# Optimization experiments

Measured on AMD Instinct MI355X. Metric: run time of the kernel, lower is better.

The kernel has to match this reference:

```python
import jax, jax.numpy as jnp
import numpy as np

B = 8            # graphs per batch
NUM_DNA = 2048   # DNA nodes per graph (equal across batch, as the module requires)
NPG = NUM_DNA + 2  # +2 contact nodes at the start of each graph
N = B * NPG
HID = 128


def _build_edges():
    # Each undirected DNA-DNA pair appears exactly once (src < dst), matching the
    # processed_pairs dedup in the torch reference. Offsets 1..4 -> ~4 couplings/node.
    rows, cols = [], []
    for b in range(B):
        base = b * NPG + 2
        for d in range(1, 5):
            i = np.arange(NUM_DNA - d)
            rows.append(base + i)
            cols.append(base + i + d)
    return np.stack([np.concatenate(rows), np.concatenate(cols)]).astype(np.int32)


def setup_inputs() -> dict:
    key = jax.random.key(0)
    ks = jax.random.split(key, 12)
    edge_index = jnp.asarray(_build_edges())          # [2, 65456]
    E = edge_index.shape[1]
    batch = jnp.repeat(jnp.arange(B, dtype=jnp.int32), NPG)  # [N]
    # contacts = first 2 nodes per graph, all-zero original features
    onf = jax.random.uniform(ks[0], (N, 4), jnp.float32) + 0.1
    contact_idx = (jnp.arange(B) * NPG)[:, None] + jnp.arange(2)[None, :]
    onf = onf.at[contact_idx.reshape(-1)].set(0.0)
    s = 1.0 / np.sqrt(HID)
    return {
        "node_features": jax.random.normal(ks[1], (N, HID), jnp.float32),
        "edge_features": jax.random.normal(ks[2], (E, HID), jnp.float32),
        "original_node_features": onf,
        "Wo1": jax.random.normal(ks[3], (HID, HID), jnp.float32) * s,
        "bo1": jax.random.normal(ks[4], (HID,), jnp.float32) * 0.01,
        "Wo2": jax.random.normal(ks[5], (HID, 1), jnp.float32) * s,
        "bo2": jax.random.normal(ks[6], (1,), jnp.float32) * 0.01,
        "Wc1": jax.random.normal(ks[7], (HID, HID), jnp.float32) * s,
        "bc1": jax.random.normal(ks[8], (HID,), jnp.float32) * 0.01,
        "Wc2": jax.random.normal(ks[9], (HID, 1), jnp.float32) * s,
        "bc2": jax.random.normal(ks[10], (1,), jnp.float32) * 0.01,
        "edge_index": edge_index,
        "batch": batch,
        "batch_size": B,
        "num_dna_nodes": NUM_DNA,
    }


def reference(node_features, edge_features, original_node_features,
              Wo1, bo1, Wo2, bo2, Wc1, bc1, Wc2, bc2,
              edge_index, batch, batch_size, num_dna_nodes):
    # Vectorized construct_hamiltonian_from_graph with n_orb = 1.
    n_orb = 1
    H_size = num_dna_nodes * n_orb
    contact = jnp.all(original_node_features == 0, axis=1)
    dna_mask = ~contact
    node_counts = jax.ops.segment_sum(jnp.ones_like(batch), batch,
                                      num_segments=batch_size)
    graph_starts = jnp.concatenate([jnp.zeros((1,), node_counts.dtype),
                                    jnp.cumsum(node_counts)[:-1]])
    # DNA node bookkeeping (contacts are the first 2 nodes of each graph)
    dna_idx = jnp.nonzero(dna_mask, size=batch_size * num_dna_nodes,
                          fill_value=0)[0]
    dna_batch = batch[dna_idx]
    dna_local = dna_idx - graph_starts[dna_batch] - 2
    # onsite MLP: Linear -> ReLU -> Linear, Hermitize (identity for n_orb=1)
    dna_feat = node_features[dna_idx]
    onsite = jax.nn.relu(dna_feat @ Wo1 + bo1) @ Wo2 + bo2      # [Nd, 1]
    coupling = jax.nn.relu(edge_features @ Wc1 + bc1) @ Wc2 + bc2  # [E, 1]
    # edge -> (graph, local row/col), upper-triangular orientation u <= v
    src, dst = edge_index[0], edge_index[1]
    eb = batch[src]
    src_loc = src - graph_starts[eb] - 2
    dst_loc = dst - graph_starts[eb] - 2
    u = jnp.minimum(src_loc, dst_loc)
    v = jnp.maximum(src_loc, dst_loc)
    valid = dna_mask[src] & dna_mask[dst] & (u != v)
    c = coupling[:, 0] * valid.astype(coupling.dtype)
    Hm = jnp.zeros((batch_size, H_size, H_size), jnp.float32)
    Hm = Hm.at[dna_batch, dna_local, dna_local].set(onsite[:, 0])
    Hm = Hm.at[eb, u, v].add(c)   # each undirected pair appears once -> add == set
    Hm = Hm.at[eb, v, u].add(c)   # Hermitian mirror (real, 1x1 blocks)
    Hm = Hm + 1e-6 * jnp.eye(H_size, dtype=Hm.dtype)
    return Hm
```

## Files before the change

### kernel.cpp

```cpp
#include <hip/hip_runtime.h>
#include <hip/hip_bf16.h>

#define HID   128
#define NPG   2050
#define HSZ   2048
#define WSTR  136

typedef __attribute__((ext_vector_type(8))) short bf16x8;
typedef __attribute__((ext_vector_type(4))) float f32x4;

union BF8 { bf16x8 v; __hip_bfloat162 h[4]; };

__device__ __forceinline__ bf16x8 cvt8(const float4 x0, const float4 x1) {
    BF8 r;
    r.h[0] = __float22bfloat162_rn(make_float2(x0.x, x0.y));
    r.h[1] = __float22bfloat162_rn(make_float2(x0.z, x0.w));
    r.h[2] = __float22bfloat162_rn(make_float2(x1.x, x1.y));
    r.h[3] = __float22bfloat162_rn(make_float2(x1.z, x1.w));
    return r.v;
}

__global__ __launch_bounds__(256) void mlp_mfma_kernel(
    const float* __restrict__ node_features,
    const float* __restrict__ edge_features,
    const float* __restrict__ Wo1, const float* __restrict__ bo1,
    const float* __restrict__ Wo2, const float* __restrict__ bo2,
    const float* __restrict__ Wc1, const float* __restrict__ bc1,
    const float* __restrict__ Wc2, const float* __restrict__ bc2,
    const int* __restrict__ edge_index, const int* __restrict__ batch,
    int node_blocks, int n_nodes, int n_edges,
    float* __restrict__ wso, float* __restrict__ wsc)
{
    __shared__ short W1t[HID * WSTR];

    const bool is_node = (blockIdx.x < (unsigned)node_blocks);
    const int  row0    = (is_node ? blockIdx.x : (blockIdx.x - node_blocks)) * HID;
    const int  nrows   = is_node ? n_nodes : n_edges;
    const float* X  = is_node ? node_features : edge_features;
    const float* W1 = is_node ? Wo1 : Wc1;
    const float* b1 = is_node ? bo1 : bc1;
    const float* W2 = is_node ? Wo2 : Wc2;
    const float* b2 = is_node ? bo2 : bc2;

    const int tid = threadIdx.x;

    {
        const int n     = tid & 127;
        const int khalf = tid >> 7;
#pragma unroll
        for (int kk = 0; kk < 16; ++kk) {
            int k0 = khalf * 64 + kk * 4;
            float a0 = W1[(k0 + 0) * HID + n];
            float a1 = W1[(k0 + 1) * HID + n];
            float a2 = W1[(k0 + 2) * HID + n];
            float a3 = W1[(k0 + 3) * HID + n];
            union { __hip_bfloat162 h[2]; short4 s; } p;
            p.h[0] = __float22bfloat162_rn(make_float2(a0, a1));
            p.h[1] = __float22bfloat162_rn(make_float2(a2, a3));
            *(short4*)&W1t[n * WSTR + k0] = p.s;
        }
    }
    __syncthreads();

    const int lane = tid & 63;
    const int wid  = tid >> 6;
    const int lr   = lane & 15;
    const int g    = lane >> 4;
    const int r0   = row0 + wid * 32;

    f32x4 acc[2][8];
#pragma unroll
    for (int rt = 0; rt < 2; ++rt)
#pragma unroll
        for (int ct = 0; ct < 8; ++ct) acc[rt][ct] = (f32x4)0.f;

    long abase[2];
    bool aok[2];
#pragma unroll
    for (int rt = 0; rt < 2; ++rt) {
        int grow = r0 + rt * 16 + lr;
        aok[rt] = (grow < nrows);
        if (is_node) {
            int gr = (grow >> 11) * NPG + 2 + (grow & (HSZ - 1));
            abase[rt] = (long)gr * HID;
        } else {
            abase[rt] = (long)grow * HID;
        }
    }

#pragma unroll
    for (int ks = 0; ks < 4; ++ks) {
        bf16x8 afr[2];
#pragma unroll
        for (int rt = 0; rt < 2; ++rt) {
            if (aok[rt]) {
                const float* p = X + abase[rt] + ks * 32 + g * 8;
                float4 x0 = *(const float4*)p;
                float4 x1 = *(const float4*)(p + 4);
                afr[rt] = cvt8(x0, x1);
            } else {
                afr[rt] = (bf16x8)0;
            }
        }
#pragma unroll
        for (int ct = 0; ct < 8; ++ct) {
            bf16x8 bfr = *(const bf16x8*)&W1t[(ct * 16 + lr) * WSTR + ks * 32 + g * 8];
            acc[0][ct] = __builtin_amdgcn_mfma_f32_16x16x32_bf16(afr[0], bfr, acc[0][ct], 0, 0, 0);
            acc[1][ct] = __builtin_amdgcn_mfma_f32_16x16x32_bf16(afr[1], bfr, acc[1][ct], 0, 0, 0);
        }
    }

    float b1v[8], w2v[8];
#pragma unroll
    for (int ct = 0; ct < 8; ++ct) {
        b1v[ct] = b1[ct * 16 + lr];
        w2v[ct] = W2[ct * 16 + lr];
    }
    const float b2s = b2[0];

#pragma unroll
    for (int rt = 0; rt < 2; ++rt) {
#pragma unroll
        for (int reg = 0; reg < 4; ++reg) {
            float p = 0.f;
#pragma unroll
            for (int ct = 0; ct < 8; ++ct) {
                float h = acc[rt][ct][reg] + b1v[ct];
                h = h > 0.f ? h : 0.f;
                p += h * w2v[ct];
            }
            p += __shfl_xor(p, 1, 64);
            p += __shfl_xor(p, 2, 64);
            p += __shfl_xor(p, 4, 64);
            p += __shfl_xor(p, 8, 64);
            if (lr == 0) {
                int grow = r0 + rt * 16 + g * 4 + reg;
                if (grow < nrows) {
                    float val = p + b2s;
                    if (is_node) {
                        wso[grow] = val;
                    } else {
                        int e   = grow;
                        int src = edge_index[e];
                        int dst = edge_index[n_edges + e];
                        int bb  = batch[src];
                        int base = bb * NPG + 2;
                        int sl = src - base, dl = dst - base;
                        int u = sl < dl ? sl : dl;
                        int v = sl < dl ? dl : sl;
                        int d = v - u;
                        if (u >= 0 && v < HSZ && d >= 1 && d <= 4) {
                            wsc[(bb * 4 + (d - 1)) * HSZ + u] = val;
                        }
                    }
                }
            }
        }
    }
}

__global__ __launch_bounds__(256) void band_write_kernel(
    const float* __restrict__ wso, const float* __restrict__ wsc,
    float* __restrict__ out, int n_rows )
{
    const int tid = threadIdx.x;
    for (int r = blockIdx.x; r < n_rows; r += gridDim.x) {
        const int b = r >> 11;
        const int l = r & (HSZ - 1);
        float4* orow = (float4*)(out + (long)r * HSZ);
#pragma unroll
        for (int half = 0; half < 2; ++half) {
            int c4 = tid + half * 256;
            int j0 = c4 << 2;
            float4 v = make_float4(0.f, 0.f, 0.f, 0.f);
            if (j0 + 3 >= l - 4 && j0 <= l + 4) {
                float e[4] = {0.f, 0.f, 0.f, 0.f};
#pragma unroll
                for (int q = 0; q < 4; ++q) {
                    int j = j0 + q;
                    if (j == l) {
                        e[q] = wso[r] + 1e-6f;
                    } else if (j > l && j <= l + 4 && j < HSZ) {
                        e[q] = wsc[(b * 4 + (j - l - 1)) * HSZ + l];
                    } else if (j < l && j >= l - 4) {
                        e[q] = wsc[(b * 4 + (l - j - 1)) * HSZ + j];
                    }
                }
                v = make_float4(e[0], e[1], e[2], e[3]);
            }
            orow[c4] = v;
        }
    }
}

extern "C" void kernel_launch(void* const* d_in, const int* in_sizes, int n_in,
                              void* d_out, int out_size, void* d_ws, size_t ws_size,
                              hipStream_t stream) {
    const float* node_features = (const float*)d_in[0];
    const float* edge_features = (const float*)d_in[1];
    const float* Wo1 = (const float*)d_in[3];
    const float* bo1 = (const float*)d_in[4];
    const float* Wo2 = (const float*)d_in[5];
    const float* bo2 = (const float*)d_in[6];
    const float* Wc1 = (const float*)d_in[7];
    const float* bc1 = (const float*)d_in[8];
    const float* Wc2 = (const float*)d_in[9];
    const float* bc2 = (const float*)d_in[10];
    const int* edge_index = (const int*)d_in[11];
    const int* batch      = (const int*)d_in[12];

    const int n_edges  = in_sizes[1] / HID;
    const int n_graphs = out_size / (HSZ * HSZ);
    const int n_dna    = n_graphs * HSZ;

    float* wso = (float*)d_ws;
    float* wsc = wso + n_dna;

    const int node_blocks = (n_dna + HID - 1) / HID;
    const int edge_blocks = (n_edges + HID - 1) / HID;
    mlp_mfma_kernel<<<node_blocks + edge_blocks, 256, 0, stream>>>(
        node_features, edge_features,
        Wo1, bo1, Wo2, bo2, Wc1, bc1, Wc2, bc2,
        edge_index, batch,
        node_blocks, n_dna, n_edges, wso, wsc);

    band_write_kernel<<<4096, 256, 0, stream>>>(wso, wsc, (float*)d_out, n_dna);
}
```

Measured before the change: 41.59 us.

## Use 512-thread blocks and issue activation loads before weight staging

Doubles the MLP block to 512 threads, so each wave handles 16 rows instead of 32, and splits the weight transpose-and-convert work across the larger block. The fp32 activation rows are now loaded into registers before the LDS weight staging and barrier, so global-load latency overlaps the weight conversion. This trades per-wave MFMA reuse of each B fragment for more waves and lower register pressure per wave. Total runtime is likely dominated by the band-write kernel's output writes, which limits any gain.

```diff
diff --git a/kernel.cpp b/kernel.cpp
--- a/kernel.cpp
+++ b/kernel.cpp
@@ -5,6 +5,7 @@
 #define NPG   2050
 #define HSZ   2048
 #define WSTR  136
+#define WELEM (HID * WSTR)
 
 typedef __attribute__((ext_vector_type(8))) short bf16x8;
 typedef __attribute__((ext_vector_type(4))) float f32x4;
@@ -20,7 +21,7 @@
     return r.v;
 }
 
-__global__ __launch_bounds__(256) void mlp_mfma_kernel(
+__global__ __launch_bounds__(512) void mlp_mfma_kernel(
     const float* __restrict__ node_features,
     const float* __restrict__ edge_features,
     const float* __restrict__ Wo1, const float* __restrict__ bo1,
@@ -31,7 +32,7 @@
     int node_blocks, int n_nodes, int n_edges,
     float* __restrict__ wso, float* __restrict__ wsc)
 {
-    __shared__ short W1t[HID * WSTR];
+    __shared__ short W1t[WELEM];
 
     const bool is_node = (blockIdx.x < (unsigned)node_blocks);
     const int  row0    = (is_node ? blockIdx.x : (blockIdx.x - node_blocks)) * HID;
@@ -42,72 +43,28 @@
     const float* W2 = is_node ? Wo2 : Wc2;
     const float* b2 = is_node ? bo2 : bc2;
 
-    const int tid = threadIdx.x;
-
-    {
-        const int n     = tid & 127;
-        const int khalf = tid >> 7;
-#pragma unroll
-        for (int kk = 0; kk < 16; ++kk) {
-            int k0 = khalf * 64 + kk * 4;
-            float a0 = W1[(k0 + 0) * HID + n];
-            float a1 = W1[(k0 + 1) * HID + n];
-            float a2 = W1[(k0 + 2) * HID + n];
-            float a3 = W1[(k0 + 3) * HID + n];
-            union { __hip_bfloat162 h[2]; short4 s; } p;
-            p.h[0] = __float22bfloat162_rn(make_float2(a0, a1));
-            p.h[1] = __float22bfloat162_rn(make_float2(a2, a3));
-            *(short4*)&W1t[n * WSTR + k0] = p.s;
-        }
-    }
-    __syncthreads();
-
+    const int tid  = threadIdx.x;
     const int lane = tid & 63;
     const int wid  = tid >> 6;
     const int lr   = lane & 15;
     const int g    = lane >> 4;
-    const int r0   = row0 + wid * 32;
-
-    f32x4 acc[2][8];
-#pragma unroll
-    for (int rt = 0; rt < 2; ++rt)
-#pragma unroll
-        for (int ct = 0; ct < 8; ++ct) acc[rt][ct] = (f32x4)0.f;
-
-    long abase[2];
-    bool aok[2];
-#pragma unroll
-    for (int rt = 0; rt < 2; ++rt) {
-        int grow = r0 + rt * 16 + lr;
-        aok[rt] = (grow < nrows);
-        if (is_node) {
-            int gr = (grow >> 11) * NPG + 2 + (grow & (HSZ - 1));
-            abase[rt] = (long)gr * HID;
-        } else {
-            abase[rt] = (long)grow * HID;
-        }
-    }
-
+    const int r0   = row0 + wid * 16;
+
+    const int grow = r0 + lr;
+    const bool aok = is_node | (grow < nrows);
+    long abase;
+    if (is_node) {
+        int gr = (grow >> 11) * NPG + 2 + (grow & (HSZ - 1));
+        abase = (long)gr * HID;
+    } else {
+        abase = aok ? (long)grow * HID : 0;
+    }
+    float4 a[8];
 #pragma unroll
     for (int ks = 0; ks < 4; ++ks) {
-        bf16x8 afr[2];
-#pragma unroll
-        for (int rt = 0; rt < 2; ++rt) {
-            if (aok[rt]) {
-                const float* p = X + abase[rt] + ks * 32 + g * 8;
-                float4 x0 = *(const float4*)p;
-                float4 x1 = *(const float4*)(p + 4);
-                afr[rt] = cvt8(x0, x1);
-            } else {
-                afr[rt] = (bf16x8)0;
-            }
-        }
-#pragma unroll
-        for (int ct = 0; ct < 8; ++ct) {
-            bf16x8 bfr = *(const bf16x8*)&W1t[(ct * 16 + lr) * WSTR + ks * 32 + g * 8];
-            acc[0][ct] = __builtin_amdgcn_mfma_f32_16x16x32_bf16(afr[0], bfr, acc[0][ct], 0, 0, 0);
-            acc[1][ct] = __builtin_amdgcn_mfma_f32_16x16x32_bf16(afr[1], bfr, acc[1][ct], 0, 0, 0);
-        }
+        const float* p = X + abase + ks * 32 + g * 8;
+        a[2 * ks + 0] = *(const float4*)p;
+        a[2 * ks + 1] = *(const float4*)(p + 4);
     }
 
     float b1v[8], w2v[8];
@@ -118,40 +75,69 @@
     }
     const float b2s = b2[0];
 
-#pragma unroll
-    for (int rt = 0; rt < 2; ++rt) {
-#pragma unroll
-        for (int reg = 0; reg < 4; ++reg) {
-            float p = 0.f;
-#pragma unroll
-            for (int ct = 0; ct < 8; ++ct) {
-                float h = acc[rt][ct][reg] + b1v[ct];
-                h = h > 0.f ? h : 0.f;
-                p += h * w2v[ct];
-            }
-            p += __shfl_xor(p, 1, 64);
-            p += __shfl_xor(p, 2, 64);
-            p += __shfl_xor(p, 4, 64);
-            p += __shfl_xor(p, 8, 64);
-            if (lr == 0) {
-                int grow = r0 + rt * 16 + g * 4 + reg;
-                if (grow < nrows) {
-                    float val = p + b2s;
-                    if (is_node) {
-                        wso[grow] = val;
-                    } else {
-                        int e   = grow;
-                        int src = edge_index[e];
-                        int dst = edge_index[n_edges + e];
-                        int bb  = batch[src];
-                        int base = bb * NPG + 2;
-                        int sl = src - base, dl = dst - base;
-                        int u = sl < dl ? sl : dl;
-                        int v = sl < dl ? dl : sl;
-                        int d = v - u;
-                        if (u >= 0 && v < HSZ && d >= 1 && d <= 4) {
-                            wsc[(bb * 4 + (d - 1)) * HSZ + u] = val;
-                        }
+    {
+        const int n  = tid & 127;
+        const int kq = tid >> 7;
+#pragma unroll
+        for (int kk = 0; kk < 8; ++kk) {
+            int k0 = kq * 32 + kk * 4;
+            float q0 = W1[(k0 + 0) * HID + n];
+            float q1 = W1[(k0 + 1) * HID + n];
+            float q2 = W1[(k0 + 2) * HID + n];
+            float q3 = W1[(k0 + 3) * HID + n];
+            union { __hip_bfloat162 h[2]; short4 s4; } p;
+            p.h[0] = __float22bfloat162_rn(make_float2(q0, q1));
+            p.h[1] = __float22bfloat162_rn(make_float2(q2, q3));
+            *(short4*)&W1t[n * WSTR + k0] = p.s4;
+        }
+    }
+    __syncthreads();
+
+    f32x4 acc[8];
+#pragma unroll
+    for (int ct = 0; ct < 8; ++ct) acc[ct] = (f32x4)0.f;
+
+#pragma unroll
+    for (int ks = 0; ks < 4; ++ks) {
+        bf16x8 afr = aok ? cvt8(a[2 * ks], a[2 * ks + 1]) : (bf16x8)0;
+#pragma unroll
+        for (int ct = 0; ct < 8; ++ct) {
+            bf16x8 bfr = *(const bf16x8*)&W1t[(ct * 16 + lr) * WSTR + ks * 32 + g * 8];
+            acc[ct] = __builtin_amdgcn_mfma_f32_16x16x32_bf16(afr, bfr, acc[ct], 0, 0, 0);
+        }
+    }
+
+#pragma unroll
+    for (int reg = 0; reg < 4; ++reg) {
+        float psum = 0.f;
+#pragma unroll
+        for (int ct = 0; ct < 8; ++ct) {
+            float h = acc[ct][reg] + b1v[ct];
+            h = h > 0.f ? h : 0.f;
+            psum += h * w2v[ct];
+        }
+        psum += __shfl_xor(psum, 1, 64);
+        psum += __shfl_xor(psum, 2, 64);
+        psum += __shfl_xor(psum, 4, 64);
+        psum += __shfl_xor(psum, 8, 64);
+        if (lr == 0) {
+            int orow = r0 + g * 4 + reg;
+            if (orow < nrows) {
+                float val = psum + b2s;
+                if (is_node) {
+                    wso[orow] = val;
+                } else {
+                    int e   = orow;
+                    int src = edge_index[e];
+                    int dst = edge_index[n_edges + e];
+                    int bb  = batch[src];
+                    int base = bb * NPG + 2;
+                    int sl = src - base, dl = dst - base;
+                    int u = sl < dl ? sl : dl;
+                    int v = sl < dl ? dl : sl;
+                    int d = v - u;
+                    if (u >= 0 && v < HSZ && d >= 1 && d <= 4) {
+                        wsc[(bb * 4 + (d - 1)) * HSZ + u] = val;
                     }
                 }
             }
@@ -218,7 +204,7 @@
 
     const int node_blocks = (n_dna + HID - 1) / HID;
     const int edge_blocks = (n_edges + HID - 1) / HID;
-    mlp_mfma_kernel<<<node_blocks + edge_blocks, 256, 0, stream>>>(
+    mlp_mfma_kernel<<<node_blocks + edge_blocks, 512, 0, stream>>>(
         node_features, edge_features,
         Wo1, bo1, Wo2, bo2, Wc1, bc1, Wc2, bc2,
         edge_index, batch,
```

Result: no change. 41.04 us (-1.3%).

## Fuse bulk zero-fill into MLP launch and patch only band entries afterward

Applied to the files above, without the earlier changes.

Adds extra blocks to the MLP kernel that zero the whole output matrix concurrently with the MLP work, and replaces the full-row band writer with a small kernel that writes only the three float4 chunks per row covering the diagonal band. This is meant to overlap the dominant output-write traffic with the MLP compute instead of serializing them. The band entries are written twice (zero then value), and the fill blocks compete with MLP blocks for CU slots.

```diff
diff --git a/kernel.cpp b/kernel.cpp
--- a/kernel.cpp
+++ b/kernel.cpp
@@ -5,6 +5,8 @@
 #define NPG   2050
 #define HSZ   2048
 #define WSTR  136
+#define WELEM (HID * WSTR)
+#define NFILL 2048
 
 typedef __attribute__((ext_vector_type(8))) short bf16x8;
 typedef __attribute__((ext_vector_type(4))) float f32x4;
@@ -20,7 +22,7 @@
     return r.v;
 }
 
-__global__ __launch_bounds__(256) void mlp_mfma_kernel(
+__global__ __launch_bounds__(256) void mlp_fill_kernel(
     const float* __restrict__ node_features,
     const float* __restrict__ edge_features,
     const float* __restrict__ Wo1, const float* __restrict__ bo1,
@@ -28,10 +30,21 @@
     const float* __restrict__ Wc1, const float* __restrict__ bc1,
     const float* __restrict__ Wc2, const float* __restrict__ bc2,
     const int* __restrict__ edge_index, const int* __restrict__ batch,
-    int node_blocks, int n_nodes, int n_edges,
-    float* __restrict__ wso, float* __restrict__ wsc)
+    int node_blocks, int mlp_blocks, int n_nodes, int n_edges,
+    float* __restrict__ wso, float* __restrict__ wsc,
+    float4* __restrict__ out4, int n4)
 {
-    __shared__ short W1t[HID * WSTR];
+    __shared__ short W1t[WELEM];
+
+    const int tid = threadIdx.x;
+
+    if (blockIdx.x >= (unsigned)mlp_blocks) {
+        int i = (blockIdx.x - mlp_blocks) * 256 + tid;
+        const int stride = NFILL * 256;
+        const float4 z = make_float4(0.f, 0.f, 0.f, 0.f);
+        for (; i < n4; i += stride) out4[i] = z;
+        return;
+    }
 
     const bool is_node = (blockIdx.x < (unsigned)node_blocks);
     const int  row0    = (is_node ? blockIdx.x : (blockIdx.x - node_blocks)) * HID;
@@ -42,22 +55,20 @@
     const float* W2 = is_node ? Wo2 : Wc2;
     const float* b2 = is_node ? bo2 : bc2;
 
-    const int tid = threadIdx.x;
-
     {
         const int n     = tid & 127;
         const int khalf = tid >> 7;
 #pragma unroll
         for (int kk = 0; kk < 16; ++kk) {
             int k0 = khalf * 64 + kk * 4;
-            float a0 = W1[(k0 + 0) * HID + n];
-            float a1 = W1[(k0 + 1) * HID + n];
-            float a2 = W1[(k0 + 2) * HID + n];
-            float a3 = W1[(k0 + 3) * HID + n];
-            union { __hip_bfloat162 h[2]; short4 s; } p;
-            p.h[0] = __float22bfloat162_rn(make_float2(a0, a1));
-            p.h[1] = __float22bfloat162_rn(make_float2(a2, a3));
-            *(short4*)&W1t[n * WSTR + k0] = p.s;
+            float q0 = W1[(k0 + 0) * HID + n];
+            float q1 = W1[(k0 + 1) * HID + n];
+            float q2 = W1[(k0 + 2) * HID + n];
+            float q3 = W1[(k0 + 3) * HID + n];
+            union { __hip_bfloat162 h[2]; short4 s4; } p;
+            p.h[0] = __float22bfloat162_rn(make_float2(q0, q1));
+            p.h[1] = __float22bfloat162_rn(make_float2(q2, q3));
+            *(short4*)&W1t[n * WSTR + k0] = p.s4;
         }
     }
     __syncthreads();
@@ -122,21 +133,21 @@
     for (int rt = 0; rt < 2; ++rt) {
 #pragma unroll
         for (int reg = 0; reg < 4; ++reg) {
-            float p = 0.f;
+            float psum = 0.f;
 #pragma unroll
             for (int ct = 0; ct < 8; ++ct) {
                 float h = acc[rt][ct][reg] + b1v[ct];
                 h = h > 0.f ? h : 0.f;
-                p += h * w2v[ct];
+                psum += h * w2v[ct];
             }
-            p += __shfl_xor(p, 1, 64);
-            p += __shfl_xor(p, 2, 64);
-            p += __shfl_xor(p, 4, 64);
-            p += __shfl_xor(p, 8, 64);
+            psum += __shfl_xor(psum, 1, 64);
+            psum += __shfl_xor(psum, 2, 64);
+            psum += __shfl_xor(psum, 4, 64);
+            psum += __shfl_xor(psum, 8, 64);
             if (lr == 0) {
                 int grow = r0 + rt * 16 + g * 4 + reg;
                 if (grow < nrows) {
-                    float val = p + b2s;
+                    float val = psum + b2s;
                     if (is_node) {
                         wso[grow] = val;
                     } else {
@@ -159,38 +170,36 @@
     }
 }
 
-__global__ __launch_bounds__(256) void band_write_kernel(
+__global__ __launch_bounds__(256) void band_patch_kernel(
     const float* __restrict__ wso, const float* __restrict__ wsc,
     float* __restrict__ out, int n_rows )
 {
-    const int tid = threadIdx.x;
-    for (int r = blockIdx.x; r < n_rows; r += gridDim.x) {
-        const int b = r >> 11;
-        const int l = r & (HSZ - 1);
-        float4* orow = (float4*)(out + (long)r * HSZ);
-#pragma unroll
-        for (int half = 0; half < 2; ++half) {
-            int c4 = tid + half * 256;
-            int j0 = c4 << 2;
-            float4 v = make_float4(0.f, 0.f, 0.f, 0.f);
-            if (j0 + 3 >= l - 4 && j0 <= l + 4) {
-                float e[4] = {0.f, 0.f, 0.f, 0.f};
-#pragma unroll
-                for (int q = 0; q < 4; ++q) {
-                    int j = j0 + q;
-                    if (j == l) {
-                        e[q] = wso[r] + 1e-6f;
-                    } else if (j > l && j <= l + 4 && j < HSZ) {
-                        e[q] = wsc[(b * 4 + (j - l - 1)) * HSZ + l];
-                    } else if (j < l && j >= l - 4) {
-                        e[q] = wsc[(b * 4 + (l - j - 1)) * HSZ + j];
-                    }
-                }
-                v = make_float4(e[0], e[1], e[2], e[3]);
-            }
-            orow[c4] = v;
-        }
-    }
+    const int t = blockIdx.x * 256 + threadIdx.x;
+    const int r = t / 3;
+    const int i = t - r * 3;
+    if (r >= n_rows) return;
+    const int b = r >> 11;
+    const int l = r & (HSZ - 1);
+    const int c4 = ((l - 4) >> 2) + i;
+    if (c4 < 0 || c4 > (HSZ / 4 - 1)) return;
+
+    float4 v = make_float4(0.f, 0.f, 0.f, 0.f);
+    const int j0 = c4 << 2;
+#pragma unroll
+    for (int q = 0; q < 4; ++q) {
+        int j   = j0 + q;
+        int dlt = j - l;
+        float e = 0.f;
+        if (dlt == 0) {
+            e = wso[r] + 1e-6f;
+        } else if (dlt >= 1 && dlt <= 4) {
+            e = wsc[(b * 4 + (dlt - 1)) * HSZ + l];
+        } else if (dlt >= -4 && dlt <= -1) {
+            e = wsc[(b * 4 + (-dlt - 1)) * HSZ + j];
+        }
+        ((float*)&v)[q] = e;
+    }
+    ((float4*)(out + (long)r * HSZ))[c4] = v;
 }
 
 extern "C" void kernel_launch(void* const* d_in, const int* in_sizes, int n_in,
@@ -218,11 +227,17 @@
 
     const int node_blocks = (n_dna + HID - 1) / HID;
     const int edge_blocks = (n_edges + HID - 1) / HID;
-    mlp_mfma_kernel<<<node_blocks + edge_blocks, 256, 0, stream>>>(
+    const int mlp_blocks  = node_blocks + edge_blocks;
+    const int n4          = out_size / 4;
+
+    mlp_fill_kernel<<<mlp_blocks + NFILL, 256, 0, stream>>>(
         node_features, edge_features,
         Wo1, bo1, Wo2, bo2, Wc1, bc1, Wc2, bc2,
         edge_index, batch,
-        node_blocks, n_dna, n_edges, wso, wsc);
-
-    band_write_kernel<<<4096, 256, 0, stream>>>(wso, wsc, (float*)d_out, n_dna);
-}
+        node_blocks, mlp_blocks, n_dna, n_edges,
+        wso, wsc, (float4*)d_out, n4);
+
+    const int patch_threads = n_dna * 3;
+    band_patch_kernel<<<(patch_threads + 255) / 256, 256, 0, stream>>>(
+        wso, wsc, (float*)d_out, n_dna);
+}
```

Result: faster. 36.87 us (-11.3%).
